# Kernel tuning notes

Measured on AMD Instinct MI355X. Metric: run time of the kernel, lower is better.

Reference implementation:

```python
import jax, jax.numpy as jnp
import numpy as np

EMBED = 128
HEADS = 4
WS = (7, 7)
N = WS[0] * WS[1]  # 49 patches per window
B_ = 8192          # batch * num_windows_total
NW = 64            # windows per image (for mask reshape)


def _rel_pos_index():
    # Deterministic relative-position index table, computed exactly as in build().
    coords = np.stack(np.meshgrid(np.arange(WS[0]), np.arange(WS[1]), indexing='ij'))
    coords = coords.reshape(2, -1)                     # [2, N]
    rel = coords[:, :, None] - coords[:, None, :]      # [2, N, N]
    rel = rel.transpose(1, 2, 0).astype(np.int64)      # [N, N, 2]
    rel[:, :, 0] += WS[0] - 1
    rel[:, :, 1] += WS[1] - 1
    rel[:, :, 0] *= 2 * WS[1] - 1
    return jnp.asarray(rel.sum(-1))                    # [N, N]

REL_IDX = _rel_pos_index()


def setup_inputs() -> dict:
    key = jax.random.key(0)
    ks = jax.random.split(key, 7)
    return {
        'x': jax.random.normal(ks[0], (B_, N, EMBED), jnp.float32),
        'mask': jax.random.normal(ks[1], (NW, N, N), jnp.float32),
        'qkv_w': jax.random.normal(ks[2], (EMBED, 3 * EMBED), jnp.float32) * 0.02,
        'qkv_b': jax.random.normal(ks[3], (3 * EMBED,), jnp.float32) * 0.02,
        'proj_w': jax.random.normal(ks[4], (EMBED, EMBED), jnp.float32) * 0.02,
        'proj_b': jax.random.normal(ks[5], (EMBED,), jnp.float32) * 0.02,
        'rel_pos_table': jax.random.normal(ks[6], ((2 * WS[0] - 1) * (2 * WS[1] - 1), HEADS), jnp.float32) * 0.02,
    }


def reference(x, mask, qkv_w, qkv_b, proj_w, proj_b, rel_pos_table):
    B, n, C = x.shape
    hd = C // HEADS
    scale = hd ** -0.5
    # qkv projection then faithful row-major reshape [B,N,3C] -> [3,B,H,N,hd]
    qkv = x @ qkv_w + qkv_b                          # [B, N, 3C]
    qkv = qkv.reshape(3, B, HEADS, n, hd)
    q, k, v = qkv[0] * scale, qkv[1], qkv[2]
    attn = jnp.einsum('bhqd,bhkd->bhqk', q, k)       # [B, H, N, N]
    # gathered relative position bias: [N*N, H] -> [H, N, N]
    bias = rel_pos_table[REL_IDX.reshape(-1)].reshape(n, n, HEADS)
    attn = attn + jnp.transpose(bias, (2, 0, 1))[None]
    # additive window mask: reshape to [B/NW, NW, H, N, N]
    attn = attn.reshape(-1, NW, HEADS, n, n) + mask[None, :, None]
    attn = attn.reshape(-1, HEADS, n, n)
    attn = jax.nn.softmax(attn, axis=-1)
    out = jnp.einsum('bhqk,bhkd->bhqd', attn, v)     # [B, H, N, hd]
    out = jnp.transpose(out, (0, 2, 1, 3)).reshape(B, n, C)
    return out @ proj_w + proj_b
```

## Files before the change

kernel.cpp:

```cpp
#include <hip/hip_runtime.h>

typedef __attribute__((ext_vector_type(8))) short short8;
typedef __attribute__((ext_vector_type(4))) float f32x4;

#define Q3 51380224

#define XB_OFF 0
#define XB_ST 136
#define Q_OFF 8704
#define QK_H 2560
#define QK_ST 40
#define K_OFF 18944
#define VT_OFF 29184
#define VT_H 2304
#define VT_ST 72
#define TRASH 38400
#define LDS_EL 38408
#define P_OFF 8704
#define P_ST 72
#define AOUT_OFF 0

__device__ __forceinline__ unsigned short f2bf(float f) {
    unsigned int u = __float_as_uint(f);
    u += 0x7FFFu + ((u >> 16) & 1u);
    return (unsigned short)(u >> 16);
}

__global__ __launch_bounds__(256) void prep(
    const float* __restrict__ qkv_w, const float* __restrict__ proj_w,
    const float* __restrict__ mask, const float* __restrict__ rpt,
    unsigned short* __restrict__ wq, unsigned short* __restrict__ pw,
    unsigned short* __restrict__ stab, float* __restrict__ T)
{
    int t = blockIdx.x * 256 + threadIdx.x;
    if (t < 49152) {
        int c = t >> 7, k = t & 127;
        wq[t] = f2bf(qkv_w[k * 384 + c]);
        return;
    }
    t -= 49152;
    if (t < 16384) {
        int c = t >> 7, k = t & 127;
        pw[t] = f2bf(proj_w[k * 128 + c]);
        return;
    }
    t -= 16384;
    if (t < 73728) {
        int R = t & 63;
        int b3 = t / (384 * 64);
        int C = (t - b3 * 384 * 64) >> 6;
        unsigned short el = TRASH;
        if (R <= 50) {
            int run = R >= 34 ? 2 : (R >= 17 ? 1 : 0);
            int sh = run == 0 ? b3 : (run == 1 ? b3 + 2 : b3 + 1);
            int offs = 128 * (sh % 3);
            int t2 = (R - run * 17) * 384 + C - offs;
            if (t2 >= 0 && t2 < 6272) {
                int h = t2 / 1568;
                int rem = t2 - h * 1568;
                int n = rem >> 5, d = rem & 31;
                el = (run == 2) ? (unsigned short)(VT_OFF + h * VT_H + d * VT_ST + n)
                   : (unsigned short)((run == 1 ? K_OFF : Q_OFF) + h * QK_H + n * QK_ST + d);
            }
        }
        stab[t] = el;
        return;
    }
    t -= 73728;
    if (t < 64 * 4 * 64 * 64) {
        int j = t & 63, i = (t >> 6) & 63, h = (t >> 12) & 3, w = t >> 14;
        float v;
        if (j >= 49) v = -1e30f;
        else if (i >= 49) v = 0.f;
        else {
            int ri = i / 7, ci = i - ri * 7, rj = j / 7, cj = j - rj * 7;
            int idx = (ri - rj + 6) * 13 + (ci - cj + 6);
            v = (rpt[idx * 4 + h] + mask[(w * 49 + i) * 49 + j]) * 1.4426950408889634f;
        }
        T[t] = v;
    }
}

__global__ __launch_bounds__(512, 4) void winattn(
    const float* __restrict__ x,
    const unsigned short* __restrict__ wq, const unsigned short* __restrict__ pw,
    const unsigned short* __restrict__ stab, const float* __restrict__ T,
    const float* __restrict__ qkv_b, const float* __restrict__ proj_b,
    float* __restrict__ out)
{
    __shared__ unsigned short lds[LDS_EL];
    unsigned int* ldsw = (unsigned int*)lds;
    const int b = blockIdx.x;
    const int tid = threadIdx.x;
    const int wid = tid >> 6;
    const int lane = tid & 63;
    const int l15 = lane & 15;
    const int lq = lane >> 4;
    const f32x4 zero = {0.f, 0.f, 0.f, 0.f};
    const float qscale = 0.17677669529663687f * 1.4426950408889634f;
    const int b3 = b % 3;

    const int base0 = b * 6272;
    const int r0_0 = base0 / 384;
    const int r0_1 = (Q3 + base0) / 384;
    const int r0_2 = (2 * Q3 + base0) / 384;

    for (int t = tid; t < 4608; t += 512) ldsw[(VT_OFF >> 1) + t] = 0u;
    for (int t = tid; t < 2400; t += 512) {
        int run = t / 300, rem = t - run * 300;
        int h = run & 3, reg = run >> 2;
        ldsw[((Q_OFF + reg * 10240 + h * QK_H + 49 * QK_ST) >> 1) + rem] = 0u;
    }

    for (int t = tid; t < 51 * 32; t += 512) {
        int row = t >> 5, kq = (t & 31) * 4;
        int run = row >= 34 ? 2 : (row >= 17 ? 1 : 0);
        int r0s = run == 2 ? r0_2 : (run == 1 ? r0_1 : r0_0);
        int gr = r0s + row - run * 17;
        float4 v = *(const float4*)&x[gr * 128 + kq];
        float sc = (row < 17) ? qscale : 1.f;
        uint2 d;
        d.x = (unsigned int)f2bf(v.x * sc) | ((unsigned int)f2bf(v.y * sc) << 16);
        d.y = (unsigned int)f2bf(v.z * sc) | ((unsigned int)f2bf(v.w * sc) << 16);
        *(uint2*)&ldsw[(row * XB_ST + kq) >> 1] = d;
    }
    __syncthreads();

    const unsigned short* stB = &stab[b3 * 384 * 64];
    for (int ntj = 0; ntj < 3; ++ntj) {
        const int C = (wid + ntj * 8) * 16 + l15;
        short8 bf[4];
        const short8* wrow = (const short8*)&wq[C * 128];
#pragma unroll
        for (int ks = 0; ks < 4; ++ks) bf[ks] = wrow[ks * 4 + lq];
        const float b1 = qkv_b[C];
        const float bq = b1 * qscale;
        const ushort4* stRow = (const ushort4*)&stB[C * 64];
#pragma unroll
        for (int mt = 0; mt < 4; ++mt) {
            f32x4 acc = zero;
#pragma unroll
            for (int ks = 0; ks < 4; ++ks) {
                short8 a = *(const short8*)&lds[(mt * 16 + l15) * XB_ST + ks * 32 + lq * 8];
                acc = __builtin_amdgcn_mfma_f32_16x16x32_bf16(a, bf[ks], acc, 0, 0, 0);
            }
            ushort4 e = stRow[mt * 4 + lq];
            int Rb = mt * 16 + lq * 4;
            lds[e.x] = f2bf(acc[0] + (Rb + 0 < 17 ? bq : b1));
            lds[e.y] = f2bf(acc[1] + (Rb + 1 < 17 ? bq : b1));
            lds[e.z] = f2bf(acc[2] + (Rb + 2 < 17 ? bq : b1));
            lds[e.w] = f2bf(acc[3] + (Rb + 3 < 17 ? bq : b1));
        }
    }
    __syncthreads();

    const int h = wid >> 1;
    {
        const int ihalf = wid & 1;
        short8 kf[4];
#pragma unroll
        for (int jt = 0; jt < 4; ++jt)
            kf[jt] = *(const short8*)&lds[K_OFF + h * QK_H + (jt * 16 + l15) * QK_ST + lq * 8];
        f32x4 acc[2][4];
#pragma unroll
        for (int it = 0; it < 2; ++it) {
            short8 qf = *(const short8*)&lds[Q_OFF + h * QK_H + (ihalf * 32 + it * 16 + l15) * QK_ST + lq * 8];
#pragma unroll
            for (int jt = 0; jt < 4; ++jt)
                acc[it][jt] = __builtin_amdgcn_mfma_f32_16x16x32_bf16(qf, kf[jt], zero, 0, 0, 0);
        }
        __syncthreads();
        const float* Tb = T + (((b & 63) * 4 + h) << 12);
#pragma unroll
        for (int it = 0; it < 2; ++it)
#pragma unroll
        for (int r = 0; r < 4; ++r) {
            int i = ihalf * 32 + it * 16 + lq * 4 + r;
            const float* Trow = Tb + i * 64 + l15;
            float s0 = acc[it][0][r] + Trow[0];
            float s1 = acc[it][1][r] + Trow[16];
            float s2 = acc[it][2][r] + Trow[32];
            float s3 = acc[it][3][r] + Trow[48];
            float m = fmaxf(fmaxf(s0, s1), fmaxf(s2, s3));
            m = fmaxf(m, __shfl_xor(m, 1));
            m = fmaxf(m, __shfl_xor(m, 2));
            m = fmaxf(m, __shfl_xor(m, 4));
            m = fmaxf(m, __shfl_xor(m, 8));
            float e0 = exp2f(s0 - m), e1 = exp2f(s1 - m);
            float e2 = exp2f(s2 - m), e3 = exp2f(s3 - m);
            float sum = e0 + e1 + e2 + e3;
            sum += __shfl_xor(sum, 1);
            sum += __shfl_xor(sum, 2);
            sum += __shfl_xor(sum, 4);
            sum += __shfl_xor(sum, 8);
            float inv = 1.f / sum;
            int pb = P_OFF + (h * 64 + i) * P_ST + l15;
            lds[pb +  0] = f2bf(e0 * inv);
            lds[pb + 16] = f2bf(e1 * inv);
            lds[pb + 32] = f2bf(e2 * inv);
            lds[pb + 48] = f2bf(e3 * inv);
        }
    }
    __syncthreads();

    {
        const int dt = wid & 1;
        const int vbase = VT_OFF + h * VT_H + (dt * 16 + l15) * VT_ST + lq * 8;
        short8 vf0 = *(const short8*)&lds[vbase];
        short8 vf1 = *(const short8*)&lds[vbase + 32];
#pragma unroll
        for (int mt = 0; mt < 4; ++mt) {
            int pbase = P_OFF + (h * 64 + mt * 16 + l15) * P_ST + lq * 8;
            short8 a0 = *(const short8*)&lds[pbase];
            short8 a1 = *(const short8*)&lds[pbase + 32];
            f32x4 acc = __builtin_amdgcn_mfma_f32_16x16x32_bf16(a0, vf0, zero, 0, 0, 0);
            acc = __builtin_amdgcn_mfma_f32_16x16x32_bf16(a1, vf1, acc, 0, 0, 0);
            int i0 = mt * 16 + lq * 4;
            int abase = AOUT_OFF + h * 32 + dt * 16 + l15;
            if (i0 + 0 < 49) lds[abase + (i0 + 0) * XB_ST] = f2bf(acc[0]);
            if (i0 + 1 < 49) lds[abase + (i0 + 1) * XB_ST] = f2bf(acc[1]);
            if (i0 + 2 < 49) lds[abase + (i0 + 2) * XB_ST] = f2bf(acc[2]);
            if (i0 + 3 < 49) lds[abase + (i0 + 3) * XB_ST] = f2bf(acc[3]);
        }
    }
    const int Cp = wid * 16 + l15;
    short8 pf[4];
#pragma unroll
    for (int ks = 0; ks < 4; ++ks)
        pf[ks] = *(const short8*)&pw[Cp * 128 + ks * 32 + lq * 8];
    const float pbv = proj_b[Cp];
    __syncthreads();

#pragma unroll
    for (int mt = 0; mt < 4; ++mt) {
        f32x4 acc = zero;
#pragma unroll
        for (int ks = 0; ks < 4; ++ks) {
            short8 a = *(const short8*)&lds[AOUT_OFF + (mt * 16 + l15) * XB_ST + ks * 32 + lq * 8];
            acc = __builtin_amdgcn_mfma_f32_16x16x32_bf16(a, pf[ks], acc, 0, 0, 0);
        }
#pragma unroll
        for (int r = 0; r < 4; ++r) {
            int R = mt * 16 + lq * 4 + r;
            if (R < 49)
                out[(b * 49 + R) * 128 + Cp] = acc[r] + pbv;
        }
    }
}

extern "C" void kernel_launch(void* const* d_in, const int* in_sizes, int n_in,
                              void* d_out, int out_size, void* d_ws, size_t ws_size,
                              hipStream_t stream) {
    const float* x      = (const float*)d_in[0];
    const float* mask   = (const float*)d_in[1];
    const float* qkv_w  = (const float*)d_in[2];
    const float* qkv_b  = (const float*)d_in[3];
    const float* proj_w = (const float*)d_in[4];
    const float* proj_b = (const float*)d_in[5];
    const float* rpt    = (const float*)d_in[6];
    float* out = (float*)d_out;

    unsigned short* wq   = (unsigned short*)d_ws;
    unsigned short* pw   = (unsigned short*)((char*)d_ws + 98304);
    unsigned short* stab = (unsigned short*)((char*)d_ws + 131072);
    float*          T    = (float*)((char*)d_ws + 278528);

    prep<<<4640, 256, 0, stream>>>(qkv_w, proj_w, mask, rpt, wq, pw, stab, T);
    winattn<<<8192, 512, 0, stream>>>(x, wq, pw, stab, T, qkv_b, proj_b, out);
}
```

Baseline: 318.8 us.

## Split QKV projection into separate GEMM kernel writing bf16 intermediate to workspace

```diff
diff --git a/kernel.cpp b/kernel.cpp
--- a/kernel.cpp
+++ b/kernel.cpp
@@ -4,6 +4,272 @@
 typedef __attribute__((ext_vector_type(4))) float f32x4;
 
 #define Q3 51380224
+#define QSCALE 0.25501654254183333f
+
+__device__ __forceinline__ unsigned short f2bf(float f) {
+    unsigned int u = __float_as_uint(f);
+    u += 0x7FFFu + ((u >> 16) & 1u);
+    return (unsigned short)(u >> 16);
+}
+
+#define WS_WQ    0
+#define WS_PW    98304
+#define WS_QMAP  131072
+#define WS_VMAP  137344
+#define WS_T     149888
+#define WS_F     4344192
+#define WS_SPLIT_NEED 312625536ULL
+
+__global__ __launch_bounds__(256) void prep_split(
+    const float* __restrict__ qkv_w, const float* __restrict__ proj_w,
+    const float* __restrict__ mask, const float* __restrict__ rpt,
+    unsigned short* __restrict__ wq, unsigned short* __restrict__ pw,
+    unsigned short* __restrict__ qmap, unsigned short* __restrict__ vmap,
+    float* __restrict__ T)
+{
+    int t = blockIdx.x * 256 + threadIdx.x;
+    if (t < 49152) {
+        int c = t >> 7, k = t & 127;
+        wq[t] = f2bf(qkv_w[k * 384 + c]);
+        return;
+    }
+    t -= 49152;
+    if (t < 16384) {
+        int c = t >> 7, k = t & 127;
+        pw[t] = f2bf(proj_w[k * 128 + c]);
+        return;
+    }
+    t -= 16384;
+    if (t < 3136) {
+        int t2 = 2 * t;
+        int h = t2 / 1568, rem = t2 - h * 1568;
+        int n = rem >> 5, d = rem & 31;
+        qmap[t] = (unsigned short)(h * 2080 + n * 40 + d);
+        return;
+    }
+    t -= 3136;
+    if (t < 6272) {
+        int h = t / 1568, rem = t - h * 1568;
+        int n = rem >> 5, d = rem & 31;
+        vmap[t] = (unsigned short)(h * 2304 + d * 72 + n);
+        return;
+    }
+    t -= 6272;
+    if (t < 64 * 4 * 64 * 64) {
+        int j = t & 63, i = (t >> 6) & 63, h = (t >> 12) & 3, w = t >> 14;
+        float v;
+        if (j >= 49) v = -1e30f;
+        else if (i >= 49) v = 0.f;
+        else {
+            int ri = i / 7, ci = i - ri * 7, rj = j / 7, cj = j - rj * 7;
+            int idx = (ri - rj + 6) * 13 + (ci - cj + 6);
+            v = (rpt[idx * 4 + h] + mask[(w * 49 + i) * 49 + j]) * 1.4426950408889634f;
+        }
+        T[t] = v;
+    }
+}
+
+__global__ __launch_bounds__(512, 8) void qkvgemm(
+    const float* __restrict__ x, const unsigned short* __restrict__ wq,
+    const float* __restrict__ qkv_b, unsigned short* __restrict__ F)
+{
+    __shared__ unsigned short xb[128 * 136];
+    unsigned int* xbw = (unsigned int*)xb;
+    const int tid = threadIdx.x;
+    const int wid = tid >> 6, lane = tid & 63;
+    const int l15 = lane & 15, lq = lane >> 4;
+    const int row0 = blockIdx.x * 128;
+    const f32x4 zero = {0.f, 0.f, 0.f, 0.f};
+
+    for (int t = tid; t < 128 * 32; t += 512) {
+        int r = t >> 5, kq = (t & 31) * 4;
+        float4 v = *(const float4*)&x[(row0 + r) * 128 + kq];
+        uint2 d;
+        d.x = (unsigned int)f2bf(v.x) | ((unsigned int)f2bf(v.y) << 16);
+        d.y = (unsigned int)f2bf(v.z) | ((unsigned int)f2bf(v.w) << 16);
+        *(uint2*)&xbw[(r * 136 + kq) >> 1] = d;
+    }
+    __syncthreads();
+
+    for (int ntj = 0; ntj < 3; ++ntj) {
+        const int C = (wid * 3 + ntj) * 16 + l15;
+        short8 bf[4];
+        const short8* wrow = (const short8*)&wq[C * 128];
+#pragma unroll
+        for (int ks = 0; ks < 4; ++ks) bf[ks] = wrow[ks * 4 + lq];
+        const float b1 = qkv_b[C];
+#pragma unroll
+        for (int mt = 0; mt < 8; ++mt) {
+            f32x4 acc = zero;
+#pragma unroll
+            for (int ks = 0; ks < 4; ++ks) {
+                short8 a = *(const short8*)&xb[(mt * 16 + l15) * 136 + ks * 32 + lq * 8];
+                acc = __builtin_amdgcn_mfma_f32_16x16x32_bf16(a, bf[ks], acc, 0, 0, 0);
+            }
+            unsigned f = (unsigned)(row0 + mt * 16 + lq * 4) * 384u + (unsigned)C;
+#pragma unroll
+            for (int r = 0; r < 4; ++r) {
+                float o = acc[r] + b1;
+                if (f < (unsigned)Q3) o *= QSCALE;
+                F[f] = f2bf(o);
+                f += 384u;
+            }
+        }
+    }
+}
+
+#define K2_K 8320
+#define K2_V 16640
+#define K2_EL 25856
+
+__global__ __launch_bounds__(512, 6) void winattn2(
+    const unsigned short* __restrict__ F, const unsigned short* __restrict__ pw,
+    const unsigned short* __restrict__ qmap, const unsigned short* __restrict__ vmap,
+    const float* __restrict__ T, const float* __restrict__ proj_b,
+    float* __restrict__ out)
+{
+    __shared__ unsigned short lds[K2_EL];
+    unsigned int* ldsw = (unsigned int*)lds;
+    const int b = blockIdx.x;
+    const int tid = threadIdx.x;
+    const int wid = tid >> 6, lane = tid & 63;
+    const int l15 = lane & 15, lq = lane >> 4;
+    const f32x4 zero = {0.f, 0.f, 0.f, 0.f};
+
+    for (int t = tid; t < 4608; t += 512) ldsw[(K2_V >> 1) + t] = 0u;
+    if (tid < 480) {
+        int tensor = tid / 240, tt = tid - tensor * 240;
+        int h = tt / 60, rem = tt - h * 60;
+        ldsw[(tensor * K2_K + h * 2080 + 1960) / 2 + rem] = 0u;
+    }
+    __syncthreads();
+
+    const unsigned short* g0 = F + (size_t)b * 6272;
+    for (int c = tid; c < 784; c += 512) {
+        uint4 v = *(const uint4*)&g0[c * 8];
+        ushort4 m = *(const ushort4*)&qmap[c * 4];
+        ldsw[m.x >> 1] = v.x; ldsw[m.y >> 1] = v.y;
+        ldsw[m.z >> 1] = v.z; ldsw[m.w >> 1] = v.w;
+    }
+    for (int c = tid; c < 784; c += 512) {
+        uint4 v = *(const uint4*)&g0[Q3 + c * 8];
+        ushort4 m = *(const ushort4*)&qmap[c * 4];
+        ldsw[(K2_K + m.x) >> 1] = v.x; ldsw[(K2_K + m.y) >> 1] = v.y;
+        ldsw[(K2_K + m.z) >> 1] = v.z; ldsw[(K2_K + m.w) >> 1] = v.w;
+    }
+    for (int c = tid; c < 784; c += 512) {
+        uint4 v = *(const uint4*)&g0[2 * (size_t)Q3 + c * 8];
+        ushort4 m0 = *(const ushort4*)&vmap[c * 8];
+        ushort4 m1 = *(const ushort4*)&vmap[c * 8 + 4];
+        lds[K2_V + m0.x] = (unsigned short)v.x; lds[K2_V + m0.y] = (unsigned short)(v.x >> 16);
+        lds[K2_V + m0.z] = (unsigned short)v.y; lds[K2_V + m0.w] = (unsigned short)(v.y >> 16);
+        lds[K2_V + m1.x] = (unsigned short)v.z; lds[K2_V + m1.y] = (unsigned short)(v.z >> 16);
+        lds[K2_V + m1.z] = (unsigned short)v.w; lds[K2_V + m1.w] = (unsigned short)(v.w >> 16);
+    }
+    __syncthreads();
+
+    const int h = wid >> 1;
+    {
+        const int ihalf = wid & 1;
+        short8 kf[4];
+#pragma unroll
+        for (int jt = 0; jt < 4; ++jt)
+            kf[jt] = *(const short8*)&lds[K2_K + h * 2080 + (jt * 16 + l15) * 40 + lq * 8];
+        f32x4 acc[2][4];
+#pragma unroll
+        for (int it = 0; it < 2; ++it) {
+            short8 qf = *(const short8*)&lds[h * 2080 + (ihalf * 32 + it * 16 + l15) * 40 + lq * 8];
+#pragma unroll
+            for (int jt = 0; jt < 4; ++jt)
+                acc[it][jt] = __builtin_amdgcn_mfma_f32_16x16x32_bf16(qf, kf[jt], zero, 0, 0, 0);
+        }
+        __syncthreads();
+        const float* Tb = T + (((b & 63) * 4 + h) << 12);
+#pragma unroll
+        for (int it = 0; it < 2; ++it)
+#pragma unroll
+        for (int r = 0; r < 4; ++r) {
+            int i = ihalf * 32 + it * 16 + lq * 4 + r;
+            const float* Trow = Tb + i * 64 + l15;
+            float s0 = acc[it][0][r] + Trow[0];
+            float s1 = acc[it][1][r] + Trow[16];
+            float s2 = acc[it][2][r] + Trow[32];
+            float s3 = acc[it][3][r] + Trow[48];
+            float m = fmaxf(fmaxf(s0, s1), fmaxf(s2, s3));
+            m = fmaxf(m, __shfl_xor(m, 1));
+            m = fmaxf(m, __shfl_xor(m, 2));
+            m = fmaxf(m, __shfl_xor(m, 4));
+            m = fmaxf(m, __shfl_xor(m, 8));
+            float e0 = exp2f(s0 - m), e1 = exp2f(s1 - m);
+            float e2 = exp2f(s2 - m), e3 = exp2f(s3 - m);
+            float sum = e0 + e1 + e2 + e3;
+            sum += __shfl_xor(sum, 1);
+            sum += __shfl_xor(sum, 2);
+            sum += __shfl_xor(sum, 4);
+            sum += __shfl_xor(sum, 8);
+            float inv = 1.f / sum;
+            if (i < 52) {
+                int pb = (h * 52 + i) * 72 + l15;
+                lds[pb +  0] = f2bf(e0 * inv);
+                lds[pb + 16] = f2bf(e1 * inv);
+                lds[pb + 32] = f2bf(e2 * inv);
+                lds[pb + 48] = f2bf(e3 * inv);
+            }
+        }
+    }
+    __syncthreads();
+
+    f32x4 accm[4];
+    const int dt = wid & 1;
+    {
+        const int vbase = K2_V + h * 2304 + (dt * 16 + l15) * 72 + lq * 8;
+        short8 vf0 = *(const short8*)&lds[vbase];
+        short8 vf1 = *(const short8*)&lds[vbase + 32];
+#pragma unroll
+        for (int mt = 0; mt < 4; ++mt) {
+            int pbase = (h * 52 + mt * 16 + l15) * 72 + lq * 8;
+            short8 a0 = *(const short8*)&lds[pbase];
+            short8 a1 = *(const short8*)&lds[pbase + 32];
+            f32x4 acc = __builtin_amdgcn_mfma_f32_16x16x32_bf16(a0, vf0, zero, 0, 0, 0);
+            accm[mt] = __builtin_amdgcn_mfma_f32_16x16x32_bf16(a1, vf1, acc, 0, 0, 0);
+        }
+    }
+    const int Cp = wid * 16 + l15;
+    short8 pf[4];
+#pragma unroll
+    for (int ks = 0; ks < 4; ++ks)
+        pf[ks] = *(const short8*)&pw[Cp * 128 + ks * 32 + lq * 8];
+    const float pbv = proj_b[Cp];
+    __syncthreads();
+    {
+        int abase = h * 32 + dt * 16 + l15;
+#pragma unroll
+        for (int mt = 0; mt < 4; ++mt) {
+            int i0 = mt * 16 + lq * 4;
+            if (i0 + 0 < 49) lds[abase + (i0 + 0) * 136] = f2bf(accm[mt][0]);
+            if (i0 + 1 < 49) lds[abase + (i0 + 1) * 136] = f2bf(accm[mt][1]);
+            if (i0 + 2 < 49) lds[abase + (i0 + 2) * 136] = f2bf(accm[mt][2]);
+            if (i0 + 3 < 49) lds[abase + (i0 + 3) * 136] = f2bf(accm[mt][3]);
+        }
+    }
+    __syncthreads();
+
+#pragma unroll
+    for (int mt = 0; mt < 4; ++mt) {
+        f32x4 acc = zero;
+#pragma unroll
+        for (int ks = 0; ks < 4; ++ks) {
+            short8 a = *(const short8*)&lds[(mt * 16 + l15) * 136 + ks * 32 + lq * 8];
+            acc = __builtin_amdgcn_mfma_f32_16x16x32_bf16(a, pf[ks], acc, 0, 0, 0);
+        }
+#pragma unroll
+        for (int r = 0; r < 4; ++r) {
+            int R = mt * 16 + lq * 4 + r;
+            if (R < 49)
+                out[(b * 49 + R) * 128 + Cp] = acc[r] + pbv;
+        }
+    }
+}
 
 #define XB_OFF 0
 #define XB_ST 136
@@ -20,30 +286,16 @@
 #define P_ST 72
 #define AOUT_OFF 0
 
-__device__ __forceinline__ unsigned short f2bf(float f) {
-    unsigned int u = __float_as_uint(f);
-    u += 0x7FFFu + ((u >> 16) & 1u);
-    return (unsigned short)(u >> 16);
-}
-
-__global__ __launch_bounds__(256) void prep(
+__global__ __launch_bounds__(256) void prep_fb(
     const float* __restrict__ qkv_w, const float* __restrict__ proj_w,
     const float* __restrict__ mask, const float* __restrict__ rpt,
     unsigned short* __restrict__ wq, unsigned short* __restrict__ pw,
     unsigned short* __restrict__ stab, float* __restrict__ T)
 {
     int t = blockIdx.x * 256 + threadIdx.x;
-    if (t < 49152) {
-        int c = t >> 7, k = t & 127;
-        wq[t] = f2bf(qkv_w[k * 384 + c]);
-        return;
-    }
+    if (t < 49152) { int c = t >> 7, k = t & 127; wq[t] = f2bf(qkv_w[k * 384 + c]); return; }
     t -= 49152;
-    if (t < 16384) {
-        int c = t >> 7, k = t & 127;
-        pw[t] = f2bf(proj_w[k * 128 + c]);
-        return;
-    }
+    if (t < 16384) { int c = t >> 7, k = t & 127; pw[t] = f2bf(proj_w[k * 128 + c]); return; }
     t -= 16384;
     if (t < 73728) {
         int R = t & 63;
@@ -56,11 +308,11 @@
             int offs = 128 * (sh % 3);
             int t2 = (R - run * 17) * 384 + C - offs;
             if (t2 >= 0 && t2 < 6272) {
-                int h = t2 / 1568;
-                int rem = t2 - h * 1568;
+                int hh = t2 / 1568;
+                int rem = t2 - hh * 1568;
                 int n = rem >> 5, d = rem & 31;
-                el = (run == 2) ? (unsigned short)(VT_OFF + h * VT_H + d * VT_ST + n)
-                   : (unsigned short)((run == 1 ? K_OFF : Q_OFF) + h * QK_H + n * QK_ST + d);
+                el = (run == 2) ? (unsigned short)(VT_OFF + hh * VT_H + d * VT_ST + n)
+                   : (unsigned short)((run == 1 ? K_OFF : Q_OFF) + hh * QK_H + n * QK_ST + d);
             }
         }
         stab[t] = el;
@@ -68,20 +320,20 @@
     }
     t -= 73728;
     if (t < 64 * 4 * 64 * 64) {
-        int j = t & 63, i = (t >> 6) & 63, h = (t >> 12) & 3, w = t >> 14;
+        int j = t & 63, i = (t >> 6) & 63, hh = (t >> 12) & 3, w = t >> 14;
         float v;
         if (j >= 49) v = -1e30f;
         else if (i >= 49) v = 0.f;
         else {
             int ri = i / 7, ci = i - ri * 7, rj = j / 7, cj = j - rj * 7;
             int idx = (ri - rj + 6) * 13 + (ci - cj + 6);
-            v = (rpt[idx * 4 + h] + mask[(w * 49 + i) * 49 + j]) * 1.4426950408889634f;
+            v = (rpt[idx * 4 + hh] + mask[(w * 49 + i) * 49 + j]) * 1.4426950408889634f;
         }
         T[t] = v;
     }
 }
 
-__global__ __launch_bounds__(512, 4) void winattn(
+__global__ __launch_bounds__(512, 4) void winattn_fb(
     const float* __restrict__ x,
     const unsigned short* __restrict__ wq, const unsigned short* __restrict__ pw,
     const unsigned short* __restrict__ stab, const float* __restrict__ T,
@@ -97,9 +349,8 @@
     const int l15 = lane & 15;
     const int lq = lane >> 4;
     const f32x4 zero = {0.f, 0.f, 0.f, 0.f};
-    const float qscale = 0.17677669529663687f * 1.4426950408889634f;
+    const float qscale = QSCALE;
     const int b3 = b % 3;
-
     const int base0 = b * 6272;
     const int r0_0 = base0 / 384;
     const int r0_1 = (Q3 + base0) / 384;
@@ -108,10 +359,9 @@
     for (int t = tid; t < 4608; t += 512) ldsw[(VT_OFF >> 1) + t] = 0u;
     for (int t = tid; t < 2400; t += 512) {
         int run = t / 300, rem = t - run * 300;
-        int h = run & 3, reg = run >> 2;
-        ldsw[((Q_OFF + reg * 10240 + h * QK_H + 49 * QK_ST) >> 1) + rem] = 0u;
-    }
-
+        int hh = run & 3, reg = run >> 2;
+        ldsw[((Q_OFF + reg * 10240 + hh * QK_H + 49 * QK_ST) >> 1) + rem] = 0u;
+    }
     for (int t = tid; t < 51 * 32; t += 512) {
         int row = t >> 5, kq = (t & 31) * 4;
         int run = row >= 34 ? 2 : (row >= 17 ? 1 : 0);
@@ -260,11 +510,22 @@
     const float* rpt    = (const float*)d_in[6];
     float* out = (float*)d_out;
 
-    unsigned short* wq   = (unsigned short*)d_ws;
-    unsigned short* pw   = (unsigned short*)((char*)d_ws + 98304);
-    unsigned short* stab = (unsigned short*)((char*)d_ws + 131072);
-    float*          T    = (float*)((char*)d_ws + 278528);
-
-    prep<<<4640, 256, 0, stream>>>(qkv_w, proj_w, mask, rpt, wq, pw, stab, T);
-    winattn<<<8192, 512, 0, stream>>>(x, wq, pw, stab, T, qkv_b, proj_b, out);
-}
+    if (ws_size >= WS_SPLIT_NEED) {
+        unsigned short* wq   = (unsigned short*)((char*)d_ws + WS_WQ);
+        unsigned short* pw   = (unsigned short*)((char*)d_ws + WS_PW);
+        unsigned short* qmap = (unsigned short*)((char*)d_ws + WS_QMAP);
+        unsigned short* vmap = (unsigned short*)((char*)d_ws + WS_VMAP);
+        float*          T    = (float*)((char*)d_ws + WS_T);
+        unsigned short* F    = (unsigned short*)((char*)d_ws + WS_F);
+        prep_split<<<4390, 256, 0, stream>>>(qkv_w, proj_w, mask, rpt, wq, pw, qmap, vmap, T);
+        qkvgemm<<<3136, 512, 0, stream>>>(x, wq, qkv_b, F);
+        winattn2<<<8192, 512, 0, stream>>>(F, pw, qmap, vmap, T, proj_b, out);
+    } else {
+        unsigned short* wq   = (unsigned short*)d_ws;
+        unsigned short* pw   = (unsigned short*)((char*)d_ws + 98304);
+        unsigned short* stab = (unsigned short*)((char*)d_ws + 131072);
+        float*          T    = (float*)((char*)d_ws + 278528);
+        prep_fb<<<4640, 256, 0, stream>>>(qkv_w, proj_w, mask, rpt, wq, pw, stab, T);
+        winattn_fb<<<8192, 512, 0, stream>>>(x, wq, pw, stab, T, qkv_b, proj_b, out);
+    }
+}
```

New measurement: 769.1 us. 2.41x slower.
